# Kernel tuning notes

Measured on AMD Instinct MI355X. Metric: run time of the kernel, lower is better.

The kernel has to match this reference:

```python
import jax, jax.numpy as jnp
import numpy as np

B, H, S, D = 4, 16, 2048, 64

def setup_inputs() -> dict:
    key = jax.random.key(0)
    kq, kk, kv = jax.random.split(key, 3)
    q = jax.random.normal(kq, (B, H, S, D), dtype=jnp.float32)
    k = jax.random.normal(kk, (B, H, S, D), dtype=jnp.float32)
    v = jax.random.normal(kv, (B, H, S, D), dtype=jnp.float32)
    # broadcastable causal mask: True = attend
    mask = jnp.tril(jnp.ones((S, S), dtype=bool))[None, None, :, :]
    return {"q": q, "k": k, "v": v, "mask": mask}

def reference(q, k, v, mask):
    # qk = einsum('... q d, ... k d -> ... q k'); mask -> -inf; softmax(qk/sqrt(d_k)); @ v
    scale = 1.0 / jnp.sqrt(jnp.asarray(q.shape[-1], q.dtype))
    scores = jnp.einsum('bhqd,bhkd->bhqk', q, k)
    scores = jnp.where(mask, scores, -jnp.inf) * scale  # -inf * scale stays -inf
    attn = jax.nn.softmax(scores, axis=-1)
    return jnp.einsum('bhqk,bhkd->bhqd', attn, v)
```

## Files before the change

kernel.cpp:

```cpp
#include <hip/hip_runtime.h>


#define SEQ 2048
#define HD  64

typedef __attribute__((ext_vector_type(8))) short short8;
typedef __attribute__((ext_vector_type(4))) float f32x4;
typedef __attribute__((ext_vector_type(2))) float f32x2;
typedef __attribute__((ext_vector_type(2))) __bf16 bf16x2;

__device__ __forceinline__ unsigned pk2(float lo, float hi) {
    union { bf16x2 v; unsigned u; } r;
    r.v = __builtin_convertvector((f32x2){lo, hi}, bf16x2);
    return r.u;
}

__global__ __launch_bounds__(256, 2) void sdpa_kernel(
    const float* __restrict__ Q, const float* __restrict__ K,
    const float* __restrict__ V, float* __restrict__ O)
{
    __shared__ __align__(16) char smraw[32768];

    const int bx = blockIdx.x;
    const int p  = bx >> 6;
    const int bh = bx & 63;

    const int tid  = threadIdx.x;
    const int lane = tid & 63;
    const int w    = tid >> 6;
    const int g    = lane >> 4;
    const int r16  = lane & 15;

    const size_t base = (size_t)bh * (SEQ * HD);

    const int k_kvo = tid >> 2;
    const int k_o   = k_kvo & 31;
    const int k_row = (k_kvo & 32) + 16 * ((k_o >> 2) & 1) + 4 * (k_o >> 3) + (k_o & 3);
    const int k_dc  = (tid & 3) * 2;
    const int v_kv0 = (tid & 31) * 2;
    const int v_db  = (tid >> 5) * 8;

    short8 ones;
    { union { short8 s; unsigned u[4]; } o_;
      o_.u[0] = o_.u[1] = o_.u[2] = o_.u[3] = 0x3F803F80u; ones = o_.s; }

    f32x4 ka0, ka1, kb0, kb1, va0, va1, vb0, vb1;

    auto LOADT = [&](int kvbase) {
        const float* kp = K + base + (size_t)(kvbase + k_kvo) * HD + k_dc * 8;
        ka0 = *(const f32x4*)(kp + 0);
        ka1 = *(const f32x4*)(kp + 4);
        kb0 = *(const f32x4*)(kp + 8);
        kb1 = *(const f32x4*)(kp + 12);
        const float* vp = V + base + (size_t)(kvbase + v_kv0) * HD + v_db;
        va0 = *(const f32x4*)(vp + 0);
        va1 = *(const f32x4*)(vp + 4);
        vb0 = *(const f32x4*)(vp + HD);
        vb1 = *(const f32x4*)(vp + HD + 4);
    };
    auto WRITET = [&](int b) {
        char* Kl = smraw + b * 16384;
        char* Vl = Kl + 8192;
        union { short8 s; unsigned u[4]; } c0, c1;
        c0.u[0] = pk2(ka0[0], ka0[1]); c0.u[1] = pk2(ka0[2], ka0[3]);
        c0.u[2] = pk2(ka1[0], ka1[1]); c0.u[3] = pk2(ka1[2], ka1[3]);
        c1.u[0] = pk2(kb0[0], kb0[1]); c1.u[1] = pk2(kb0[2], kb0[3]);
        c1.u[2] = pk2(kb1[0], kb1[1]); c1.u[3] = pk2(kb1[2], kb1[3]);
        const int r7 = k_row & 7;
        *(short8*)(Kl + ((k_row * 8 + (k_dc ^ r7)) << 4))       = c0.s;
        *(short8*)(Kl + ((k_row * 8 + ((k_dc + 1) ^ r7)) << 4)) = c1.s;
        const int u  = v_kv0 >> 3;
        const int wo = (v_kv0 & 7) * 2;
        #pragma unroll
        for (int i = 0; i < 4; ++i) {
            const int d = v_db + i;
            *(unsigned*)(Vl + ((d * 8 + (u ^ (d & 7))) << 4) + wo) = pk2(va0[i], vb0[i]);
        }
        #pragma unroll
        for (int i = 0; i < 4; ++i) {
            const int d = v_db + 4 + i;
            *(unsigned*)(Vl + ((d * 8 + (u ^ (d & 7))) << 4) + wo) = pk2(va1[i], vb1[i]);
        }
    };

    const float SC = 0.18033688011112042f;

    #pragma unroll 1
    for (int tile = 0; tile < 2; ++tile) {
        const int qbase = (tile == 0 ? 15 - p : p) * 128;
        const int wq = qbase + w * 32;

        short8 qf[2][2];
        #pragma unroll
        for (int qs = 0; qs < 2; ++qs) {
            const float* qp = Q + base + (size_t)(wq + qs * 16 + r16) * HD + 8 * g;
            #pragma unroll
            for (int c = 0; c < 2; ++c) {
                f32x4 a = *(const f32x4*)(qp + c * 32);
                f32x4 b = *(const f32x4*)(qp + c * 32 + 4);
                union { short8 s; unsigned u[4]; } t;
                t.u[0] = pk2(a[0] * SC, a[1] * SC);
                t.u[1] = pk2(a[2] * SC, a[3] * SC);
                t.u[2] = pk2(b[0] * SC, b[1] * SC);
                t.u[3] = pk2(b[2] * SC, b[3] * SC);
                qf[qs][c] = t.s;
            }
        }

        f32x4 oacc[2][4] = {};
        f32x4 lacc[2] = {};
        float mrun[2] = {-1e30f, -1e30f};

        const int nkvb = (qbase + 128) >> 6;

        __syncthreads();
        LOADT(0);
        WRITET(0);
        __syncthreads();

        for (int kvb = 0; kvb < nkvb; ++kvb) {
            const int kvbase = kvb << 6;
            const int buf = kvb & 1;
            const bool more = (kvb + 1 < nkvb);

            if (more) LOADT((kvb + 1) << 6);

            if (kvbase <= wq + 31) {
                const char* Kl = smraw + buf * 16384;
                const char* Vl = Kl + 8192;

                f32x4 sa[2][2][2];
                #pragma unroll
                for (int qs = 0; qs < 2; ++qs)
                    #pragma unroll
                    for (int c2 = 0; c2 < 2; ++c2)
                        #pragma unroll
                        for (int t = 0; t < 2; ++t)
                            sa[qs][c2][t] = (f32x4){0.f, 0.f, 0.f, 0.f};
                __builtin_amdgcn_s_setprio(1);
                #pragma unroll
                for (int c2 = 0; c2 < 2; ++c2)
                    #pragma unroll
                    for (int t = 0; t < 2; ++t)
                        #pragma unroll
                        for (int c = 0; c < 2; ++c) {
                            const int row = c2 * 32 + t * 16 + r16;
                            short8 kf = *(const short8*)(Kl + ((row * 8 + ((4 * c + g) ^ (row & 7))) << 4));
                            sa[0][c2][t] = __builtin_amdgcn_mfma_f32_16x16x32_bf16(kf, qf[0][c], sa[0][c2][t], 0, 0, 0);
                            sa[1][c2][t] = __builtin_amdgcn_mfma_f32_16x16x32_bf16(kf, qf[1][c], sa[1][c2][t], 0, 0, 0);
                        }
                __builtin_amdgcn_s_setprio(0);

                #pragma unroll
                for (int qs = 0; qs < 2; ++qs) {
                    const int q0 = wq + qs * 16;
                    if (kvbase + 63 > q0) {
                        const int qrow = q0 + r16;
                        #pragma unroll
                        for (int c2 = 0; c2 < 2; ++c2)
                            #pragma unroll
                            for (int t = 0; t < 2; ++t)
                                #pragma unroll
                                for (int r = 0; r < 4; ++r) {
                                    const int kv = kvbase + c2 * 32 + 8 * g + 4 * t + r;
                                    if (kv > qrow) sa[qs][c2][t][r] = -1e30f;
                                }
                    }
                }

                float mnew[2];
                #pragma unroll
                for (int qs = 0; qs < 2; ++qs) {
                    float mloc = sa[qs][0][0][0];
                    #pragma unroll
                    for (int c2 = 0; c2 < 2; ++c2)
                        #pragma unroll
                        for (int t = 0; t < 2; ++t)
                            #pragma unroll
                            for (int r = 0; r < 4; ++r)
                                mloc = fmaxf(mloc, sa[qs][c2][t][r]);
                    mloc = fmaxf(mloc, __shfl_xor(mloc, 16));
                    mloc = fmaxf(mloc, __shfl_xor(mloc, 32));
                    mnew[qs] = fmaxf(mrun[qs], mloc);
                }
                if (!__all((mnew[0] - mrun[0] <= 8.0f) && (mnew[1] - mrun[1] <= 8.0f))) {
                    #pragma unroll
                    for (int qs = 0; qs < 2; ++qs) {
                        const float alpha = __builtin_amdgcn_exp2f(mrun[qs] - mnew[qs]);
                        mrun[qs] = mnew[qs];
                        lacc[qs][0] *= alpha;
                        #pragma unroll
                        for (int dt = 0; dt < 4; ++dt) oacc[qs][dt] *= alpha;
                    }
                }
                #pragma unroll
                for (int qs = 0; qs < 2; ++qs)
                    #pragma unroll
                    for (int c2 = 0; c2 < 2; ++c2)
                        #pragma unroll
                        for (int t = 0; t < 2; ++t)
                            #pragma unroll
                            for (int r = 0; r < 4; ++r)
                                sa[qs][c2][t][r] =
                                    __builtin_amdgcn_exp2f(sa[qs][c2][t][r] - mrun[qs]);

                #pragma unroll
                for (int c2 = 0; c2 < 2; ++c2) {
                    union { short8 s; unsigned u[4]; } pf0, pf1;
                    pf0.u[0] = pk2(sa[0][c2][0][0], sa[0][c2][0][1]);
                    pf0.u[1] = pk2(sa[0][c2][0][2], sa[0][c2][0][3]);
                    pf0.u[2] = pk2(sa[0][c2][1][0], sa[0][c2][1][1]);
                    pf0.u[3] = pk2(sa[0][c2][1][2], sa[0][c2][1][3]);
                    pf1.u[0] = pk2(sa[1][c2][0][0], sa[1][c2][0][1]);
                    pf1.u[1] = pk2(sa[1][c2][0][2], sa[1][c2][0][3]);
                    pf1.u[2] = pk2(sa[1][c2][1][0], sa[1][c2][1][1]);
                    pf1.u[3] = pk2(sa[1][c2][1][2], sa[1][c2][1][3]);
                    __builtin_amdgcn_s_setprio(1);
                    lacc[0] = __builtin_amdgcn_mfma_f32_16x16x32_bf16(ones, pf0.s, lacc[0], 0, 0, 0);
                    lacc[1] = __builtin_amdgcn_mfma_f32_16x16x32_bf16(ones, pf1.s, lacc[1], 0, 0, 0);
                    #pragma unroll
                    for (int dt = 0; dt < 4; ++dt) {
                        const int row = dt * 16 + r16;
                        short8 vf = *(const short8*)(Vl + ((row * 8 + ((c2 * 4 + g) ^ (row & 7))) << 4));
                        oacc[0][dt] = __builtin_amdgcn_mfma_f32_16x16x32_bf16(vf, pf0.s, oacc[0][dt], 0, 0, 0);
                        oacc[1][dt] = __builtin_amdgcn_mfma_f32_16x16x32_bf16(vf, pf1.s, oacc[1][dt], 0, 0, 0);
                    }
                    __builtin_amdgcn_s_setprio(0);
                }
            }

            if (more) {
                WRITET(buf ^ 1);
                __syncthreads();
            }
        }

        #pragma unroll
        for (int qs = 0; qs < 2; ++qs) {
            const float inv = 1.0f / lacc[qs][0];
            float* op = O + base + (size_t)(wq + qs * 16 + r16) * HD + 4 * g;
            #pragma unroll
            for (int dt = 0; dt < 4; ++dt) {
                f32x4 vv = oacc[qs][dt] * inv;
                *(f32x4*)(op + dt * 16) = vv;
            }
        }
    }
}

extern "C" void kernel_launch(void* const* d_in, const int* in_sizes, int n_in,
                              void* d_out, int out_size, void* d_ws, size_t ws_size,
                              hipStream_t stream) {
    (void)in_sizes; (void)n_in; (void)out_size; (void)d_ws; (void)ws_size;
    const float* q = (const float*)d_in[0];
    const float* k = (const float*)d_in[1];
    const float* v = (const float*)d_in[2];
    float* o = (float*)d_out;
    sdpa_kernel<<<dim3(64 * 8), dim3(256), 0, stream>>>(q, k, v, o);
}
```

Measured before the change: 183.7 us.

## Halve the per-block query tile to 64 rows and double the block count

```diff
diff --git a/kernel.cpp b/kernel.cpp
--- a/kernel.cpp
+++ b/kernel.cpp
@@ -15,7 +15,7 @@
     return r.u;
 }
 
-__global__ __launch_bounds__(256, 2) void sdpa_kernel(
+__global__ __launch_bounds__(256, 4) void sdpa_kernel(
     const float* __restrict__ Q, const float* __restrict__ K,
     const float* __restrict__ V, float* __restrict__ O)
 {
@@ -87,13 +87,12 @@
 
     #pragma unroll 1
     for (int tile = 0; tile < 2; ++tile) {
-        const int qbase = (tile == 0 ? 15 - p : p) * 128;
-        const int wq = qbase + w * 32;
-
-        short8 qf[2][2];
-        #pragma unroll
-        for (int qs = 0; qs < 2; ++qs) {
-            const float* qp = Q + base + (size_t)(wq + qs * 16 + r16) * HD + 8 * g;
+        const int qbase = (tile == 0 ? 31 - p : p) * 64;
+        const int wq = qbase + w * 16;
+
+        short8 qf[2];
+        {
+            const float* qp = Q + base + (size_t)(wq + r16) * HD + 8 * g;
             #pragma unroll
             for (int c = 0; c < 2; ++c) {
                 f32x4 a = *(const f32x4*)(qp + c * 32);
@@ -103,15 +102,15 @@
                 t.u[1] = pk2(a[2] * SC, a[3] * SC);
                 t.u[2] = pk2(b[0] * SC, b[1] * SC);
                 t.u[3] = pk2(b[2] * SC, b[3] * SC);
-                qf[qs][c] = t.s;
-            }
-        }
-
-        f32x4 oacc[2][4] = {};
-        f32x4 lacc[2] = {};
-        float mrun[2] = {-1e30f, -1e30f};
-
-        const int nkvb = (qbase + 128) >> 6;
+                qf[c] = t.s;
+            }
+        }
+
+        f32x4 oacc[4] = {};
+        f32x4 lacc = {};
+        float mrun = -1e30f;
+
+        const int nkvb = (qbase + 64) >> 6;
 
         __syncthreads();
         LOADT(0);
@@ -125,18 +124,16 @@
 
             if (more) LOADT((kvb + 1) << 6);
 
-            if (kvbase <= wq + 31) {
+            if (kvbase <= wq + 15) {
                 const char* Kl = smraw + buf * 16384;
                 const char* Vl = Kl + 8192;
 
-                f32x4 sa[2][2][2];
-                #pragma unroll
-                for (int qs = 0; qs < 2; ++qs)
-                    #pragma unroll
-                    for (int c2 = 0; c2 < 2; ++c2)
-                        #pragma unroll
-                        for (int t = 0; t < 2; ++t)
-                            sa[qs][c2][t] = (f32x4){0.f, 0.f, 0.f, 0.f};
+                f32x4 sa[2][2];
+                #pragma unroll
+                for (int c2 = 0; c2 < 2; ++c2)
+                    #pragma unroll
+                    for (int t = 0; t < 2; ++t)
+                        sa[c2][t] = (f32x4){0.f, 0.f, 0.f, 0.f};
                 __builtin_amdgcn_s_setprio(1);
                 #pragma unroll
                 for (int c2 = 0; c2 < 2; ++c2)
@@ -146,84 +143,63 @@
                         for (int c = 0; c < 2; ++c) {
                             const int row = c2 * 32 + t * 16 + r16;
                             short8 kf = *(const short8*)(Kl + ((row * 8 + ((4 * c + g) ^ (row & 7))) << 4));
-                            sa[0][c2][t] = __builtin_amdgcn_mfma_f32_16x16x32_bf16(kf, qf[0][c], sa[0][c2][t], 0, 0, 0);
-                            sa[1][c2][t] = __builtin_amdgcn_mfma_f32_16x16x32_bf16(kf, qf[1][c], sa[1][c2][t], 0, 0, 0);
+                            sa[c2][t] = __builtin_amdgcn_mfma_f32_16x16x32_bf16(kf, qf[c], sa[c2][t], 0, 0, 0);
                         }
                 __builtin_amdgcn_s_setprio(0);
 
-                #pragma unroll
-                for (int qs = 0; qs < 2; ++qs) {
-                    const int q0 = wq + qs * 16;
-                    if (kvbase + 63 > q0) {
-                        const int qrow = q0 + r16;
-                        #pragma unroll
-                        for (int c2 = 0; c2 < 2; ++c2)
-                            #pragma unroll
-                            for (int t = 0; t < 2; ++t)
-                                #pragma unroll
-                                for (int r = 0; r < 4; ++r) {
-                                    const int kv = kvbase + c2 * 32 + 8 * g + 4 * t + r;
-                                    if (kv > qrow) sa[qs][c2][t][r] = -1e30f;
-                                }
-                    }
-                }
-
-                float mnew[2];
-                #pragma unroll
-                for (int qs = 0; qs < 2; ++qs) {
-                    float mloc = sa[qs][0][0][0];
+                if (kvbase + 63 > wq) {
+                    const int qrow = wq + r16;
                     #pragma unroll
                     for (int c2 = 0; c2 < 2; ++c2)
                         #pragma unroll
                         for (int t = 0; t < 2; ++t)
                             #pragma unroll
-                            for (int r = 0; r < 4; ++r)
-                                mloc = fmaxf(mloc, sa[qs][c2][t][r]);
-                    mloc = fmaxf(mloc, __shfl_xor(mloc, 16));
-                    mloc = fmaxf(mloc, __shfl_xor(mloc, 32));
-                    mnew[qs] = fmaxf(mrun[qs], mloc);
+                            for (int r = 0; r < 4; ++r) {
+                                const int kv = kvbase + c2 * 32 + 8 * g + 4 * t + r;
+                                if (kv > qrow) sa[c2][t][r] = -1e30f;
+                            }
                 }
-                if (!__all((mnew[0] - mrun[0] <= 8.0f) && (mnew[1] - mrun[1] <= 8.0f))) {
-                    #pragma unroll
-                    for (int qs = 0; qs < 2; ++qs) {
-                        const float alpha = __builtin_amdgcn_exp2f(mrun[qs] - mnew[qs]);
-                        mrun[qs] = mnew[qs];
-                        lacc[qs][0] *= alpha;
-                        #pragma unroll
-                        for (int dt = 0; dt < 4; ++dt) oacc[qs][dt] *= alpha;
-                    }
+
+                float mloc = sa[0][0][0];
+                #pragma unroll
+                for (int c2 = 0; c2 < 2; ++c2)
+                    #pragma unroll
+                    for (int t = 0; t < 2; ++t)
+                        #pragma unroll
+                        for (int r = 0; r < 4; ++r)
+                            mloc = fmaxf(mloc, sa[c2][t][r]);
+                mloc = fmaxf(mloc, __shfl_xor(mloc, 16));
+                mloc = fmaxf(mloc, __shfl_xor(mloc, 32));
+                const float mnew = fmaxf(mrun, mloc);
+                if (!__all(mnew - mrun <= 8.0f)) {
+                    const float alpha = __builtin_amdgcn_exp2f(mrun - mnew);
+                    mrun = mnew;
+                    lacc[0] *= alpha;
+                    #pragma unroll
+                    for (int dt = 0; dt < 4; ++dt) oacc[dt] *= alpha;
                 }
                 #pragma unroll
-                for (int qs = 0; qs < 2; ++qs)
-                    #pragma unroll
-                    for (int c2 = 0; c2 < 2; ++c2)
-                        #pragma unroll
-                        for (int t = 0; t < 2; ++t)
-                            #pragma unroll
-                            for (int r = 0; r < 4; ++r)
-                                sa[qs][c2][t][r] =
-                                    __builtin_amdgcn_exp2f(sa[qs][c2][t][r] - mrun[qs]);
+                for (int c2 = 0; c2 < 2; ++c2)
+                    #pragma unroll
+                    for (int t = 0; t < 2; ++t)
+                        #pragma unroll
+                        for (int r = 0; r < 4; ++r)
+                            sa[c2][t][r] = __builtin_amdgcn_exp2f(sa[c2][t][r] - mrun);
 
                 #pragma unroll
                 for (int c2 = 0; c2 < 2; ++c2) {
-                    union { short8 s; unsigned u[4]; } pf0, pf1;
-                    pf0.u[0] = pk2(sa[0][c2][0][0], sa[0][c2][0][1]);
-                    pf0.u[1] = pk2(sa[0][c2][0][2], sa[0][c2][0][3]);
-                    pf0.u[2] = pk2(sa[0][c2][1][0], sa[0][c2][1][1]);
-                    pf0.u[3] = pk2(sa[0][c2][1][2], sa[0][c2][1][3]);
-                    pf1.u[0] = pk2(sa[1][c2][0][0], sa[1][c2][0][1]);
-                    pf1.u[1] = pk2(sa[1][c2][0][2], sa[1][c2][0][3]);
-                    pf1.u[2] = pk2(sa[1][c2][1][0], sa[1][c2][1][1]);
-                    pf1.u[3] = pk2(sa[1][c2][1][2], sa[1][c2][1][3]);
+                    union { short8 s; unsigned u[4]; } pf;
+                    pf.u[0] = pk2(sa[c2][0][0], sa[c2][0][1]);
+                    pf.u[1] = pk2(sa[c2][0][2], sa[c2][0][3]);
+                    pf.u[2] = pk2(sa[c2][1][0], sa[c2][1][1]);
+                    pf.u[3] = pk2(sa[c2][1][2], sa[c2][1][3]);
                     __builtin_amdgcn_s_setprio(1);
-                    lacc[0] = __builtin_amdgcn_mfma_f32_16x16x32_bf16(ones, pf0.s, lacc[0], 0, 0, 0);
-                    lacc[1] = __builtin_amdgcn_mfma_f32_16x16x32_bf16(ones, pf1.s, lacc[1], 0, 0, 0);
+                    lacc = __builtin_amdgcn_mfma_f32_16x16x32_bf16(ones, pf.s, lacc, 0, 0, 0);
                     #pragma unroll
                     for (int dt = 0; dt < 4; ++dt) {
                         const int row = dt * 16 + r16;
                         short8 vf = *(const short8*)(Vl + ((row * 8 + ((c2 * 4 + g) ^ (row & 7))) << 4));
-                        oacc[0][dt] = __builtin_amdgcn_mfma_f32_16x16x32_bf16(vf, pf0.s, oacc[0][dt], 0, 0, 0);
-                        oacc[1][dt] = __builtin_amdgcn_mfma_f32_16x16x32_bf16(vf, pf1.s, oacc[1][dt], 0, 0, 0);
+                        oacc[dt] = __builtin_amdgcn_mfma_f32_16x16x32_bf16(vf, pf.s, oacc[dt], 0, 0, 0);
                     }
                     __builtin_amdgcn_s_setprio(0);
                 }
@@ -235,13 +211,12 @@
             }
         }
 
-        #pragma unroll
-        for (int qs = 0; qs < 2; ++qs) {
-            const float inv = 1.0f / lacc[qs][0];
-            float* op = O + base + (size_t)(wq + qs * 16 + r16) * HD + 4 * g;
+        {
+            const float inv = 1.0f / lacc[0];
+            float* op = O + base + (size_t)(wq + r16) * HD + 4 * g;
             #pragma unroll
             for (int dt = 0; dt < 4; ++dt) {
-                f32x4 vv = oacc[qs][dt] * inv;
+                f32x4 vv = oacc[dt] * inv;
                 *(f32x4*)(op + dt * 16) = vv;
             }
         }
@@ -256,5 +231,5 @@
     const float* k = (const float*)d_in[1];
     const float* v = (const float*)d_in[2];
     float* o = (float*)d_out;
-    sdpa_kernel<<<dim3(64 * 8), dim3(256), 0, stream>>>(q, k, v, o);
+    sdpa_kernel<<<dim3(64 * 16), dim3(256), 0, stream>>>(q, k, v, o);
 }
```

New measurement: 260.4 us. 1.42x slower.

## Use 512-thread blocks with 256-row query tiles instead of paired 128-row tiles

Applied to the files above, without the earlier changes.

```diff
diff --git a/kernel.cpp b/kernel.cpp
--- a/kernel.cpp
+++ b/kernel.cpp
@@ -15,60 +15,54 @@
     return r.u;
 }
 
-__global__ __launch_bounds__(256, 2) void sdpa_kernel(
+__global__ __launch_bounds__(512, 4) void sdpa_kernel(
     const float* __restrict__ Q, const float* __restrict__ K,
     const float* __restrict__ V, float* __restrict__ O)
 {
     __shared__ __align__(16) char smraw[32768];
 
     const int bx = blockIdx.x;
-    const int p  = bx >> 6;
     const int bh = bx & 63;
+    const int qt = (bx < 256) ? (7 - (bx >> 6)) : ((bx - 256) >> 6);
+    const int qbase = qt * 256;
 
     const int tid  = threadIdx.x;
     const int lane = tid & 63;
     const int w    = tid >> 6;
     const int g    = lane >> 4;
     const int r16  = lane & 15;
+    const int wq   = qbase + w * 32;
 
     const size_t base = (size_t)bh * (SEQ * HD);
 
-    const int k_kvo = tid >> 2;
+    const int k_kvo = tid >> 3;
+    const int k_u   = tid & 7;
     const int k_o   = k_kvo & 31;
     const int k_row = (k_kvo & 32) + 16 * ((k_o >> 2) & 1) + 4 * (k_o >> 3) + (k_o & 3);
-    const int k_dc  = (tid & 3) * 2;
     const int v_kv0 = (tid & 31) * 2;
-    const int v_db  = (tid >> 5) * 8;
+    const int v_db  = (tid >> 5) * 4;
 
     short8 ones;
     { union { short8 s; unsigned u[4]; } o_;
       o_.u[0] = o_.u[1] = o_.u[2] = o_.u[3] = 0x3F803F80u; ones = o_.s; }
 
-    f32x4 ka0, ka1, kb0, kb1, va0, va1, vb0, vb1;
+    f32x4 ka0, ka1, va0, vb0;
 
     auto LOADT = [&](int kvbase) {
-        const float* kp = K + base + (size_t)(kvbase + k_kvo) * HD + k_dc * 8;
+        const float* kp = K + base + (size_t)(kvbase + k_kvo) * HD + k_u * 8;
         ka0 = *(const f32x4*)(kp + 0);
         ka1 = *(const f32x4*)(kp + 4);
-        kb0 = *(const f32x4*)(kp + 8);
-        kb1 = *(const f32x4*)(kp + 12);
         const float* vp = V + base + (size_t)(kvbase + v_kv0) * HD + v_db;
         va0 = *(const f32x4*)(vp + 0);
-        va1 = *(const f32x4*)(vp + 4);
         vb0 = *(const f32x4*)(vp + HD);
-        vb1 = *(const f32x4*)(vp + HD + 4);
     };
     auto WRITET = [&](int b) {
         char* Kl = smraw + b * 16384;
         char* Vl = Kl + 8192;
-        union { short8 s; unsigned u[4]; } c0, c1;
+        union { short8 s; unsigned u[4]; } c0;
         c0.u[0] = pk2(ka0[0], ka0[1]); c0.u[1] = pk2(ka0[2], ka0[3]);
         c0.u[2] = pk2(ka1[0], ka1[1]); c0.u[3] = pk2(ka1[2], ka1[3]);
-        c1.u[0] = pk2(kb0[0], kb0[1]); c1.u[1] = pk2(kb0[2], kb0[3]);
-        c1.u[2] = pk2(kb1[0], kb1[1]); c1.u[3] = pk2(kb1[2], kb1[3]);
-        const int r7 = k_row & 7;
-        *(short8*)(Kl + ((k_row * 8 + (k_dc ^ r7)) << 4))       = c0.s;
-        *(short8*)(Kl + ((k_row * 8 + ((k_dc + 1) ^ r7)) << 4)) = c1.s;
+        *(short8*)(Kl + ((k_row * 8 + (k_u ^ (k_row & 7))) << 4)) = c0.s;
         const int u  = v_kv0 >> 3;
         const int wo = (v_kv0 & 7) * 2;
         #pragma unroll
@@ -76,174 +70,162 @@
             const int d = v_db + i;
             *(unsigned*)(Vl + ((d * 8 + (u ^ (d & 7))) << 4) + wo) = pk2(va0[i], vb0[i]);
         }
+    };
+
+    const float SC = 0.18033688011112042f;
+
+    short8 qf[2][2];
+    #pragma unroll
+    for (int qs = 0; qs < 2; ++qs) {
+        const float* qp = Q + base + (size_t)(wq + qs * 16 + r16) * HD + 8 * g;
         #pragma unroll
-        for (int i = 0; i < 4; ++i) {
-            const int d = v_db + 4 + i;
-            *(unsigned*)(Vl + ((d * 8 + (u ^ (d & 7))) << 4) + wo) = pk2(va1[i], vb1[i]);
-        }
-    };
-
-    const float SC = 0.18033688011112042f;
-
-    #pragma unroll 1
-    for (int tile = 0; tile < 2; ++tile) {
-        const int qbase = (tile == 0 ? 15 - p : p) * 128;
-        const int wq = qbase + w * 32;
-
-        short8 qf[2][2];
-        #pragma unroll
-        for (int qs = 0; qs < 2; ++qs) {
-            const float* qp = Q + base + (size_t)(wq + qs * 16 + r16) * HD + 8 * g;
-            #pragma unroll
-            for (int c = 0; c < 2; ++c) {
-                f32x4 a = *(const f32x4*)(qp + c * 32);
-                f32x4 b = *(const f32x4*)(qp + c * 32 + 4);
-                union { short8 s; unsigned u[4]; } t;
-                t.u[0] = pk2(a[0] * SC, a[1] * SC);
-                t.u[1] = pk2(a[2] * SC, a[3] * SC);
-                t.u[2] = pk2(b[0] * SC, b[1] * SC);
-                t.u[3] = pk2(b[2] * SC, b[3] * SC);
-                qf[qs][c] = t.s;
-            }
-        }
-
-        f32x4 oacc[2][4] = {};
-        f32x4 lacc[2] = {};
-        float mrun[2] = {-1e30f, -1e30f};
-
-        const int nkvb = (qbase + 128) >> 6;
-
-        __syncthreads();
-        LOADT(0);
-        WRITET(0);
-        __syncthreads();
-
-        for (int kvb = 0; kvb < nkvb; ++kvb) {
-            const int kvbase = kvb << 6;
-            const int buf = kvb & 1;
-            const bool more = (kvb + 1 < nkvb);
-
-            if (more) LOADT((kvb + 1) << 6);
-
-            if (kvbase <= wq + 31) {
-                const char* Kl = smraw + buf * 16384;
-                const char* Vl = Kl + 8192;
-
-                f32x4 sa[2][2][2];
-                #pragma unroll
-                for (int qs = 0; qs < 2; ++qs)
-                    #pragma unroll
-                    for (int c2 = 0; c2 < 2; ++c2)
-                        #pragma unroll
-                        for (int t = 0; t < 2; ++t)
-                            sa[qs][c2][t] = (f32x4){0.f, 0.f, 0.f, 0.f};
-                __builtin_amdgcn_s_setprio(1);
+        for (int c = 0; c < 2; ++c) {
+            f32x4 a = *(const f32x4*)(qp + c * 32);
+            f32x4 b = *(const f32x4*)(qp + c * 32 + 4);
+            union { short8 s; unsigned u[4]; } t;
+            t.u[0] = pk2(a[0] * SC, a[1] * SC);
+            t.u[1] = pk2(a[2] * SC, a[3] * SC);
+            t.u[2] = pk2(b[0] * SC, b[1] * SC);
+            t.u[3] = pk2(b[2] * SC, b[3] * SC);
+            qf[qs][c] = t.s;
+        }
+    }
+
+    f32x4 oacc[2][4] = {};
+    f32x4 lacc[2] = {};
+    float mrun[2] = {-1e30f, -1e30f};
+
+    const int nkvb = (qbase + 256) >> 6;
+
+    LOADT(0);
+    WRITET(0);
+    __syncthreads();
+
+    for (int kvb = 0; kvb < nkvb; ++kvb) {
+        const int kvbase = kvb << 6;
+        const int buf = kvb & 1;
+        const bool more = (kvb + 1 < nkvb);
+
+        if (more) LOADT((kvb + 1) << 6);
+
+        if (kvbase <= wq + 31) {
+            const char* Kl = smraw + buf * 16384;
+            const char* Vl = Kl + 8192;
+
+            f32x4 sa[2][2][2];
+            #pragma unroll
+            for (int qs = 0; qs < 2; ++qs)
                 #pragma unroll
                 for (int c2 = 0; c2 < 2; ++c2)
                     #pragma unroll
                     for (int t = 0; t < 2; ++t)
-                        #pragma unroll
-                        for (int c = 0; c < 2; ++c) {
-                            const int row = c2 * 32 + t * 16 + r16;
-                            short8 kf = *(const short8*)(Kl + ((row * 8 + ((4 * c + g) ^ (row & 7))) << 4));
-                            sa[0][c2][t] = __builtin_amdgcn_mfma_f32_16x16x32_bf16(kf, qf[0][c], sa[0][c2][t], 0, 0, 0);
-                            sa[1][c2][t] = __builtin_amdgcn_mfma_f32_16x16x32_bf16(kf, qf[1][c], sa[1][c2][t], 0, 0, 0);
-                        }
-                __builtin_amdgcn_s_setprio(0);
-
-                #pragma unroll
-                for (int qs = 0; qs < 2; ++qs) {
-                    const int q0 = wq + qs * 16;
-                    if (kvbase + 63 > q0) {
-                        const int qrow = q0 + r16;
-                        #pragma unroll
-                        for (int c2 = 0; c2 < 2; ++c2)
-                            #pragma unroll
-                            for (int t = 0; t < 2; ++t)
-                                #pragma unroll
-                                for (int r = 0; r < 4; ++r) {
-                                    const int kv = kvbase + c2 * 32 + 8 * g + 4 * t + r;
-                                    if (kv > qrow) sa[qs][c2][t][r] = -1e30f;
-                                }
+                        sa[qs][c2][t] = (f32x4){0.f, 0.f, 0.f, 0.f};
+            __builtin_amdgcn_s_setprio(1);
+            #pragma unroll
+            for (int c2 = 0; c2 < 2; ++c2)
+                #pragma unroll
+                for (int t = 0; t < 2; ++t)
+                    #pragma unroll
+                    for (int c = 0; c < 2; ++c) {
+                        const int row = c2 * 32 + t * 16 + r16;
+                        short8 kf = *(const short8*)(Kl + ((row * 8 + ((4 * c + g) ^ (row & 7))) << 4));
+                        sa[0][c2][t] = __builtin_amdgcn_mfma_f32_16x16x32_bf16(kf, qf[0][c], sa[0][c2][t], 0, 0, 0);
+                        sa[1][c2][t] = __builtin_amdgcn_mfma_f32_16x16x32_bf16(kf, qf[1][c], sa[1][c2][t], 0, 0, 0);
                     }
-                }
-
-                float mnew[2];
-                #pragma unroll
-                for (int qs = 0; qs < 2; ++qs) {
-                    float mloc = sa[qs][0][0][0];
+            __builtin_amdgcn_s_setprio(0);
+
+            #pragma unroll
+            for (int qs = 0; qs < 2; ++qs) {
+                const int q0 = wq + qs * 16;
+                if (kvbase + 63 > q0) {
+                    const int qrow = q0 + r16;
                     #pragma unroll
                     for (int c2 = 0; c2 < 2; ++c2)
                         #pragma unroll
                         for (int t = 0; t < 2; ++t)
                             #pragma unroll
-                            for (int r = 0; r < 4; ++r)
-                                mloc = fmaxf(mloc, sa[qs][c2][t][r]);
-                    mloc = fmaxf(mloc, __shfl_xor(mloc, 16));
-                    mloc = fmaxf(mloc, __shfl_xor(mloc, 32));
-                    mnew[qs] = fmaxf(mrun[qs], mloc);
+                            for (int r = 0; r < 4; ++r) {
+                                const int kv = kvbase + c2 * 32 + 8 * g + 4 * t + r;
+                                if (kv > qrow) sa[qs][c2][t][r] = -1e30f;
+                            }
                 }
-                if (!__all((mnew[0] - mrun[0] <= 8.0f) && (mnew[1] - mrun[1] <= 8.0f))) {
-                    #pragma unroll
-                    for (int qs = 0; qs < 2; ++qs) {
-                        const float alpha = __builtin_amdgcn_exp2f(mrun[qs] - mnew[qs]);
-                        mrun[qs] = mnew[qs];
-                        lacc[qs][0] *= alpha;
+            }
+
+            float mnew[2];
+            #pragma unroll
+            for (int qs = 0; qs < 2; ++qs) {
+                float mloc = sa[qs][0][0][0];
+                #pragma unroll
+                for (int c2 = 0; c2 < 2; ++c2)
+                    #pragma unroll
+                    for (int t = 0; t < 2; ++t)
                         #pragma unroll
-                        for (int dt = 0; dt < 4; ++dt) oacc[qs][dt] *= alpha;
-                    }
+                        for (int r = 0; r < 4; ++r)
+                            mloc = fmaxf(mloc, sa[qs][c2][t][r]);
+                mloc = fmaxf(mloc, __shfl_xor(mloc, 16));
+                mloc = fmaxf(mloc, __shfl_xor(mloc, 32));
+                mnew[qs] = fmaxf(mrun[qs], mloc);
+            }
+            if (!__all((mnew[0] - mrun[0] <= 8.0f) && (mnew[1] - mrun[1] <= 8.0f))) {
+                #pragma unroll
+                for (int qs = 0; qs < 2; ++qs) {
+                    const float alpha = __builtin_amdgcn_exp2f(mrun[qs] - mnew[qs]);
+                    mrun[qs] = mnew[qs];
+                    lacc[qs][0] *= alpha;
+                    #pragma unroll
+                    for (int dt = 0; dt < 4; ++dt) oacc[qs][dt] *= alpha;
                 }
-                #pragma unroll
-                for (int qs = 0; qs < 2; ++qs)
-                    #pragma unroll
-                    for (int c2 = 0; c2 < 2; ++c2)
+            }
+            #pragma unroll
+            for (int qs = 0; qs < 2; ++qs)
+                #pragma unroll
+                for (int c2 = 0; c2 < 2; ++c2)
+                    #pragma unroll
+                    for (int t = 0; t < 2; ++t)
                         #pragma unroll
-                        for (int t = 0; t < 2; ++t)
-                            #pragma unroll
-                            for (int r = 0; r < 4; ++r)
-                                sa[qs][c2][t][r] =
-                                    __builtin_amdgcn_exp2f(sa[qs][c2][t][r] - mrun[qs]);
-
-                #pragma unroll
-                for (int c2 = 0; c2 < 2; ++c2) {
-                    union { short8 s; unsigned u[4]; } pf0, pf1;
-                    pf0.u[0] = pk2(sa[0][c2][0][0], sa[0][c2][0][1]);
-                    pf0.u[1] = pk2(sa[0][c2][0][2], sa[0][c2][0][3]);
-                    pf0.u[2] = pk2(sa[0][c2][1][0], sa[0][c2][1][1]);
-                    pf0.u[3] = pk2(sa[0][c2][1][2], sa[0][c2][1][3]);
-                    pf1.u[0] = pk2(sa[1][c2][0][0], sa[1][c2][0][1]);
-                    pf1.u[1] = pk2(sa[1][c2][0][2], sa[1][c2][0][3]);
-                    pf1.u[2] = pk2(sa[1][c2][1][0], sa[1][c2][1][1]);
-                    pf1.u[3] = pk2(sa[1][c2][1][2], sa[1][c2][1][3]);
-                    __builtin_amdgcn_s_setprio(1);
-                    lacc[0] = __builtin_amdgcn_mfma_f32_16x16x32_bf16(ones, pf0.s, lacc[0], 0, 0, 0);
-                    lacc[1] = __builtin_amdgcn_mfma_f32_16x16x32_bf16(ones, pf1.s, lacc[1], 0, 0, 0);
-                    #pragma unroll
-                    for (int dt = 0; dt < 4; ++dt) {
-                        const int row = dt * 16 + r16;
-                        short8 vf = *(const short8*)(Vl + ((row * 8 + ((c2 * 4 + g) ^ (row & 7))) << 4));
-                        oacc[0][dt] = __builtin_amdgcn_mfma_f32_16x16x32_bf16(vf, pf0.s, oacc[0][dt], 0, 0, 0);
-                        oacc[1][dt] = __builtin_amdgcn_mfma_f32_16x16x32_bf16(vf, pf1.s, oacc[1][dt], 0, 0, 0);
-                    }
-                    __builtin_amdgcn_s_setprio(0);
+                        for (int r = 0; r < 4; ++r)
+                            sa[qs][c2][t][r] =
+                                __builtin_amdgcn_exp2f(sa[qs][c2][t][r] - mrun[qs]);
+
+            #pragma unroll
+            for (int c2 = 0; c2 < 2; ++c2) {
+                union { short8 s; unsigned u[4]; } pf0, pf1;
+                pf0.u[0] = pk2(sa[0][c2][0][0], sa[0][c2][0][1]);
+                pf0.u[1] = pk2(sa[0][c2][0][2], sa[0][c2][0][3]);
+                pf0.u[2] = pk2(sa[0][c2][1][0], sa[0][c2][1][1]);
+                pf0.u[3] = pk2(sa[0][c2][1][2], sa[0][c2][1][3]);
+                pf1.u[0] = pk2(sa[1][c2][0][0], sa[1][c2][0][1]);
+                pf1.u[1] = pk2(sa[1][c2][0][2], sa[1][c2][0][3]);
+                pf1.u[2] = pk2(sa[1][c2][1][0], sa[1][c2][1][1]);
+                pf1.u[3] = pk2(sa[1][c2][1][2], sa[1][c2][1][3]);
+                __builtin_amdgcn_s_setprio(1);
+                lacc[0] = __builtin_amdgcn_mfma_f32_16x16x32_bf16(ones, pf0.s, lacc[0], 0, 0, 0);
+                lacc[1] = __builtin_amdgcn_mfma_f32_16x16x32_bf16(ones, pf1.s, lacc[1], 0, 0, 0);
+                #pragma unroll
+                for (int dt = 0; dt < 4; ++dt) {
+                    const int row = dt * 16 + r16;
+                    short8 vf = *(const short8*)(Vl + ((row * 8 + ((c2 * 4 + g) ^ (row & 7))) << 4));
+                    oacc[0][dt] = __builtin_amdgcn_mfma_f32_16x16x32_bf16(vf, pf0.s, oacc[0][dt], 0, 0, 0);
+                    oacc[1][dt] = __builtin_amdgcn_mfma_f32_16x16x32_bf16(vf, pf1.s, oacc[1][dt], 0, 0, 0);
                 }
-            }
-
-            if (more) {
-                WRITET(buf ^ 1);
-                __syncthreads();
-            }
-        }
-
+                __builtin_amdgcn_s_setprio(0);
+            }
+        }
+
+        if (more) {
+            WRITET(buf ^ 1);
+            __syncthreads();
+        }
+    }
+
+    #pragma unroll
+    for (int qs = 0; qs < 2; ++qs) {
+        const float inv = 1.0f / lacc[qs][0];
+        float* op = O + base + (size_t)(wq + qs * 16 + r16) * HD + 4 * g;
         #pragma unroll
-        for (int qs = 0; qs < 2; ++qs) {
-            const float inv = 1.0f / lacc[qs][0];
-            float* op = O + base + (size_t)(wq + qs * 16 + r16) * HD + 4 * g;
-            #pragma unroll
-            for (int dt = 0; dt < 4; ++dt) {
-                f32x4 vv = oacc[qs][dt] * inv;
-                *(f32x4*)(op + dt * 16) = vv;
-            }
+        for (int dt = 0; dt < 4; ++dt) {
+            f32x4 vv = oacc[qs][dt] * inv;
+            *(f32x4*)(op + dt * 16) = vv;
         }
     }
 }
@@ -256,5 +238,5 @@
     const float* k = (const float*)d_in[1];
     const float* v = (const float*)d_in[2];
     float* o = (float*)d_out;
-    sdpa_kernel<<<dim3(64 * 8), dim3(256), 0, stream>>>(q, k, v, o);
+    sdpa_kernel<<<dim3(512), dim3(512), 0, stream>>>(q, k, v, o);
 }
```

Result: slower. 290.0 us (+57.9%).
